# Kernel tuning notes

Hardware: AMD Instinct MI355X
Metric: run time of the kernel (lower is better)

The kernel has to match this reference:

```python
import jax, jax.numpy as jnp
import numpy as np
from functools import partial

BLUR_K = 5
SIGMA = 1.5
DOWN = 4
SCALE = 5.0
OFFSET = 0.2

_DN = ('NCHW', 'OIHW', 'NCHW')


def _gaussian_kernel(k, sigma):
    x = jnp.arange(k, dtype=jnp.float32) - (k - 1) / 2.0
    g = jnp.exp(-x ** 2 / (2.0 * sigma ** 2))
    g2 = jnp.outer(g, g)
    g2 = g2 / g2.sum()
    return g2.reshape(1, 1, k, k)


def setup_inputs() -> dict:
    key = jax.random.key(0)
    left_rgb = jax.random.uniform(key, (16, 3, 544, 960), dtype=jnp.float32)
    return {"left_rgb": left_rgb}


def reference(left_rgb):
    B, C, H, W = left_rgb.shape
    # rgb -> gray (1x1 conv with fixed weights)
    w = jnp.array([0.2989, 0.587, 0.114], dtype=left_rgb.dtype)
    gray = jnp.einsum('bchw,c->bhw', left_rgb, w)[:, None]  # [B,1,H,W]

    # gaussian blur with reflect padding (torch F.pad mode='reflect')
    pad = BLUR_K // 2
    gray_p = jnp.pad(gray, ((0, 0), (0, 0), (pad, pad), (pad, pad)), mode='reflect')
    gk = _gaussian_kernel(BLUR_K, SIGMA).astype(left_rgb.dtype)
    gray_smooth = jax.lax.conv_general_dilated(gray_p, gk, (1, 1), 'VALID',
                                               dimension_numbers=_DN)

    # sobel gradients (cross-correlation, zero padding=1, same as torch conv2d)
    sx = jnp.array([[-1., 0., 1.], [-2., 0., 2.], [-1., 0., 1.]],
                   dtype=left_rgb.dtype).reshape(1, 1, 3, 3)
    sy = jnp.array([[-1., -2., -1.], [0., 0., 0.], [1., 2., 1.]],
                   dtype=left_rgb.dtype).reshape(1, 1, 3, 3)
    gx = jax.lax.conv_general_dilated(gray_smooth, sx, (1, 1), [(1, 1), (1, 1)],
                                      dimension_numbers=_DN)
    gy = jax.lax.conv_general_dilated(gray_smooth, sy, (1, 1), [(1, 1), (1, 1)],
                                      dimension_numbers=_DN)
    mag = jnp.sqrt(gx ** 2 + gy ** 2 + 1e-6)  # [B,1,H,W]

    # avg_pool2d kernel=stride=DOWN (H, W divisible by DOWN)
    down = mag.reshape(B, 1, H // DOWN, DOWN, W // DOWN, DOWN).mean(axis=(3, 5))

    edge_mask = jax.nn.sigmoid(SCALE * (down - OFFSET)) ** 2.0
    return edge_mask
```

## Files before the change

kernel.cpp:

```cpp
#include <hip/hip_runtime.h>
#include <cmath>

constexpr int B = 16, C = 3, H = 544, W = 960;
constexpr int OH = 136, OW = 240;
constexpr size_t HW = (size_t)H * W;

constexpr int TRW = 17;
constexpr int TCW = 30;
constexpr int NTILES = B * TRW * TCW;
constexpr int WPB = 4;
constexpr int NBLK = NTILES / WPB;
constexpr int CPX = NBLK / 8;

constexpr int GRr = 38;
constexpr int GQ = 10;
constexpr int NQ = GRr * GQ;
constexpr int GS2 = 44;

__global__ __launch_bounds__(256)
void edge_wave(const float* __restrict__ in, float* __restrict__ out,
               float gn0, float gn1, float gn2)
{
    __shared__ float gray[WPB * GRr * GS2];

    const int tid  = threadIdx.x;
    const int lane = tid & 63;
    const int wv   = tid >> 6;
    const int blk  = ((int)blockIdx.x & 7) * CPX + ((int)blockIdx.x >> 3);
    const int t    = blk * WPB + wv;
    const int tc   = t % TCW;
    const int tr   = (t / TCW) % TRW;
    const int b    = t / (TCW * TRW);
    const int mh0  = tr * 32, mw0 = tc * 32;
    const float* inb = in + (size_t)b * C * HW;
    float* gw = &gray[wv * GRr * GS2];

    auto qaddr = [&](int q) -> const float* {
        const int r = q / GQ, cq = q - r * GQ;
        int g = mh0 - 3 + r;
        g = g < 0 ? -g : (g >= H ? 2 * H - 2 - g : g);
        int gcb = mw0 - 4 + 4 * cq;
        gcb = gcb < 0 ? 0 : (gcb > W - 4 ? W - 4 : gcb);
        return inb + (size_t)g * W + gcb;
    };
    auto cvt = [&](const float4& R, const float4& G, const float4& Bc) -> float4 {
        float4 g;
        g.x = fmaf(0.2989f, R.x, fmaf(0.587f, G.x, 0.114f * Bc.x));
        g.y = fmaf(0.2989f, R.y, fmaf(0.587f, G.y, 0.114f * Bc.y));
        g.z = fmaf(0.2989f, R.z, fmaf(0.587f, G.z, 0.114f * Bc.z));
        g.w = fmaf(0.2989f, R.w, fmaf(0.587f, G.w, 0.114f * Bc.w));
        return g;
    };

    {
        float4 Rv[3], Gv[3], Bv[3];
        #pragma unroll
        for (int k = 0; k < 3; ++k) {
            const float* p = qaddr(lane + 64 * k);
            Rv[k] = *reinterpret_cast<const float4*>(p);
            Gv[k] = *reinterpret_cast<const float4*>(p + HW);
            Bv[k] = *reinterpret_cast<const float4*>(p + 2 * HW);
        }
        #pragma unroll
        for (int k = 0; k < 3; ++k) {
            const int q = lane + 64 * k;
            const int r = q / GQ, cq = q - r * GQ;
            *reinterpret_cast<float4*>(&gw[r * GS2 + 4 * cq]) = cvt(Rv[k], Gv[k], Bv[k]);
        }
    }
    {
        float4 Rv[3], Gv[3], Bv[3];
        int qk[3];
        #pragma unroll
        for (int k = 0; k < 3; ++k) {
            int q = lane + 192 + 64 * k;
            qk[k] = q;
            q = q < NQ ? q : NQ - 1;
            const float* p = qaddr(q);
            Rv[k] = *reinterpret_cast<const float4*>(p);
            Gv[k] = *reinterpret_cast<const float4*>(p + HW);
            Bv[k] = *reinterpret_cast<const float4*>(p + 2 * HW);
        }
        #pragma unroll
        for (int k = 0; k < 3; ++k) {
            const int q = qk[k];
            if (q < NQ) {
                const int r = q / GQ, cq = q - r * GQ;
                *reinterpret_cast<float4*>(&gw[r * GS2 + 4 * cq]) = cvt(Rv[k], Gv[k], Bv[k]);
            }
        }
    }

    asm volatile("s_waitcnt lgkmcnt(0)" ::: "memory");
    __builtin_amdgcn_sched_barrier(0);

    if (tc == 0) {
        if (lane < GRr) {
            float* g_ = &gw[lane * GS2];
            const float4 v = make_float4(g_[8], g_[7], g_[6], g_[5]);
            *reinterpret_cast<float4*>(g_) = v;
        }
    } else if (tc == TCW - 1) {
        if (lane < GRr) {
            float* g_ = &gw[lane * GS2];
            const float4 v = make_float4(g_[34], g_[33], g_[32], g_[31]);
            *reinterpret_cast<float4*>(&g_[36]) = v;
        }
    }
    asm volatile("s_waitcnt lgkmcnt(0)" ::: "memory");
    __builtin_amdgcn_sched_barrier(0);

    __builtin_amdgcn_s_setprio(1);
    {
        const int or_ = lane >> 3;
        const int oc  = lane & 7;
        const int rb  = 4 * or_;
        const int lc0 = 4 * oc;

        float sm6[6][6];
        #pragma unroll
        for (int i = 0; i < 6; ++i)
            #pragma unroll
            for (int j = 0; j < 6; ++j) sm6[i][j] = 0.f;

        const float gk[5] = {gn0, gn1, gn2, gn1, gn0};
        #pragma unroll
        for (int t2 = 0; t2 < 10; ++t2) {
            const float* p = &gw[(rb + t2) * GS2 + lc0];
            const float4 u = *reinterpret_cast<const float4*>(p);
            const float4 v = *reinterpret_cast<const float4*>(p + 4);
            const float4 w = *reinterpret_cast<const float4*>(p + 8);
            const float t12[12] = {u.x, u.y, u.z, u.w, v.x, v.y, v.z, v.w,
                                   w.x, w.y, w.z, w.w};
            float h6[6];
            #pragma unroll
            for (int j = 0; j < 6; ++j)
                h6[j] = fmaf(gn0, t12[1 + j] + t12[5 + j],
                        fmaf(gn1, t12[2 + j] + t12[4 + j], gn2 * t12[3 + j]));
            #pragma unroll
            for (int i = 0; i < 6; ++i) {
                const int m = t2 - i;
                if (m >= 0 && m < 5) {
                    #pragma unroll
                    for (int j = 0; j < 6; ++j)
                        sm6[i][j] = fmaf(gk[m], h6[j], sm6[i][j]);
                }
            }
        }

        #pragma unroll
        for (int i = 0; i < 6; ++i) {
            const int hh = mh0 + 4 * or_ - 1 + i;
            const float rm = (hh >= 0 && hh < H) ? 1.f : 0.f;
            #pragma unroll
            for (int j = 0; j < 6; ++j) {
                const int ww = mw0 + 4 * oc - 1 + j;
                sm6[i][j] *= rm * ((ww >= 0 && ww < W) ? 1.f : 0.f);
            }
        }

        float acc[4] = {0.f, 0.f, 0.f, 0.f};
        #pragma unroll
        for (int i = 0; i < 4; ++i) {
            #pragma unroll
            for (int j = 0; j < 4; ++j) {
                const float a00 = sm6[i][j],     a01 = sm6[i][j + 1],     a02 = sm6[i][j + 2];
                const float a10 = sm6[i + 1][j],                          a12 = sm6[i + 1][j + 2];
                const float a20 = sm6[i + 2][j], a21 = sm6[i + 2][j + 1], a22 = sm6[i + 2][j + 2];
                const float gx = (a02 - a00) + 2.f * (a12 - a10) + (a22 - a20);
                const float gy = (a20 + 2.f * a21 + a22) - (a00 + 2.f * a01 + a02);
                acc[i] += sqrtf(gx * gx + gy * gy + 1e-6f);
            }
        }
        const float down = ((acc[0] + acc[1]) + (acc[2] + acc[3])) * (1.f / 16.f);
        const float x = 5.0f * (down - 0.2f);
        const float sg = 1.f / (1.f + __expf(-x));
        out[((size_t)b * OH + 8 * tr + or_) * OW + 8 * tc + oc] = sg * sg;
    }
    __builtin_amdgcn_s_setprio(0);
}

extern "C" void kernel_launch(void* const* d_in, const int* in_sizes, int n_in,
                              void* d_out, int out_size, void* d_ws, size_t ws_size,
                              hipStream_t stream) {
    const float* in = (const float*)d_in[0];
    float* out = (float*)d_out;

    const double g0 = std::exp(-4.0 / 4.5);
    const double g1 = std::exp(-1.0 / 4.5);
    const double g2 = 1.0;
    const double S = 2.0 * (g0 + g1) + g2;
    const float gn0 = (float)(g0 / S);
    const float gn1 = (float)(g1 / S);
    const float gn2 = (float)(g2 / S);

    hipLaunchKernelGGL(edge_wave, dim3(NBLK), dim3(256), 0, stream,
                       in, out, gn0, gn1, gn2);
}
```

Baseline: 31.01 us.

## Widen per-wave tile to 32x64 with two output pixels per lane

Each wave now covers a 32x64 input tile instead of 32x32, and each lane computes two horizontally adjacent pooled outputs, written as a single float2 store. The halo overhead per output shrinks, horizontal blur intermediates are shared across the two outputs, and all 11 load batches are issued before conversion, giving more memory-level parallelism. In exchange the block drops to 128 threads (2 waves), register pressure rises with the wider accumulators and 33 in-flight float4 loads, and occupancy may fall.

```diff
diff --git a/kernel.cpp b/kernel.cpp
--- a/kernel.cpp
+++ b/kernel.cpp
@@ -6,18 +6,19 @@
 constexpr size_t HW = (size_t)H * W;
 
 constexpr int TRW = 17;
-constexpr int TCW = 30;
+constexpr int TCW = 15;
 constexpr int NTILES = B * TRW * TCW;
-constexpr int WPB = 4;
+constexpr int WPB = 2;
 constexpr int NBLK = NTILES / WPB;
 constexpr int CPX = NBLK / 8;
 
 constexpr int GRr = 38;
-constexpr int GQ = 10;
+constexpr int GQ = 18;
 constexpr int NQ = GRr * GQ;
-constexpr int GS2 = 44;
+constexpr int GS2 = 76;
+constexpr int NLD = 11;
 
-__global__ __launch_bounds__(256)
+__global__ __launch_bounds__(128)
 void edge_wave(const float* __restrict__ in, float* __restrict__ out,
                float gn0, float gn1, float gn2)
 {
@@ -31,7 +32,7 @@
     const int tc   = t % TCW;
     const int tr   = (t / TCW) % TRW;
     const int b    = t / (TCW * TRW);
-    const int mh0  = tr * 32, mw0 = tc * 32;
+    const int mh0  = tr * 32, mw0 = tc * 64;
     const float* inb = in + (size_t)b * C * HW;
     float* gw = &gray[wv * GRr * GS2];
 
@@ -43,51 +44,28 @@
         gcb = gcb < 0 ? 0 : (gcb > W - 4 ? W - 4 : gcb);
         return inb + (size_t)g * W + gcb;
     };
-    auto cvt = [&](const float4& R, const float4& G, const float4& Bc) -> float4 {
-        float4 g;
-        g.x = fmaf(0.2989f, R.x, fmaf(0.587f, G.x, 0.114f * Bc.x));
-        g.y = fmaf(0.2989f, R.y, fmaf(0.587f, G.y, 0.114f * Bc.y));
-        g.z = fmaf(0.2989f, R.z, fmaf(0.587f, G.z, 0.114f * Bc.z));
-        g.w = fmaf(0.2989f, R.w, fmaf(0.587f, G.w, 0.114f * Bc.w));
-        return g;
-    };
 
-    {
-        float4 Rv[3], Gv[3], Bv[3];
-        #pragma unroll
-        for (int k = 0; k < 3; ++k) {
-            const float* p = qaddr(lane + 64 * k);
-            Rv[k] = *reinterpret_cast<const float4*>(p);
-            Gv[k] = *reinterpret_cast<const float4*>(p + HW);
-            Bv[k] = *reinterpret_cast<const float4*>(p + 2 * HW);
-        }
-        #pragma unroll
-        for (int k = 0; k < 3; ++k) {
-            const int q = lane + 64 * k;
+    float4 Rv[NLD], Gv[NLD], Bv[NLD];
+    #pragma unroll
+    for (int k = 0; k < NLD; ++k) {
+        int q = lane + 64 * k;
+        q = q < NQ ? q : NQ - 1;
+        const float* p = qaddr(q);
+        Rv[k] = *reinterpret_cast<const float4*>(p);
+        Gv[k] = *reinterpret_cast<const float4*>(p + HW);
+        Bv[k] = *reinterpret_cast<const float4*>(p + 2 * HW);
+    }
+    #pragma unroll
+    for (int k = 0; k < NLD; ++k) {
+        const int q = lane + 64 * k;
+        if (q < NQ) {
             const int r = q / GQ, cq = q - r * GQ;
-            *reinterpret_cast<float4*>(&gw[r * GS2 + 4 * cq]) = cvt(Rv[k], Gv[k], Bv[k]);
-        }
-    }
-    {
-        float4 Rv[3], Gv[3], Bv[3];
-        int qk[3];
-        #pragma unroll
-        for (int k = 0; k < 3; ++k) {
-            int q = lane + 192 + 64 * k;
-            qk[k] = q;
-            q = q < NQ ? q : NQ - 1;
-            const float* p = qaddr(q);
-            Rv[k] = *reinterpret_cast<const float4*>(p);
-            Gv[k] = *reinterpret_cast<const float4*>(p + HW);
-            Bv[k] = *reinterpret_cast<const float4*>(p + 2 * HW);
-        }
-        #pragma unroll
-        for (int k = 0; k < 3; ++k) {
-            const int q = qk[k];
-            if (q < NQ) {
-                const int r = q / GQ, cq = q - r * GQ;
-                *reinterpret_cast<float4*>(&gw[r * GS2 + 4 * cq]) = cvt(Rv[k], Gv[k], Bv[k]);
-            }
+            float4 g;
+            g.x = fmaf(0.2989f, Rv[k].x, fmaf(0.587f, Gv[k].x, 0.114f * Bv[k].x));
+            g.y = fmaf(0.2989f, Rv[k].y, fmaf(0.587f, Gv[k].y, 0.114f * Bv[k].y));
+            g.z = fmaf(0.2989f, Rv[k].z, fmaf(0.587f, Gv[k].z, 0.114f * Bv[k].z));
+            g.w = fmaf(0.2989f, Rv[k].w, fmaf(0.587f, Gv[k].w, 0.114f * Bv[k].w));
+            *reinterpret_cast<float4*>(&gw[r * GS2 + 4 * cq]) = g;
         }
     }
 
@@ -103,8 +81,8 @@
     } else if (tc == TCW - 1) {
         if (lane < GRr) {
             float* g_ = &gw[lane * GS2];
-            const float4 v = make_float4(g_[34], g_[33], g_[32], g_[31]);
-            *reinterpret_cast<float4*>(&g_[36]) = v;
+            const float4 v = make_float4(g_[66], g_[65], g_[64], g_[63]);
+            *reinterpret_cast<float4*>(&g_[68]) = v;
         }
     }
     asm volatile("s_waitcnt lgkmcnt(0)" ::: "memory");
@@ -113,15 +91,15 @@
     __builtin_amdgcn_s_setprio(1);
     {
         const int or_ = lane >> 3;
-        const int oc  = lane & 7;
+        const int ocp = lane & 7;
         const int rb  = 4 * or_;
-        const int lc0 = 4 * oc;
+        const int lc0 = 8 * ocp;
 
-        float sm6[6][6];
+        float sm6[6][10];
         #pragma unroll
         for (int i = 0; i < 6; ++i)
             #pragma unroll
-            for (int j = 0; j < 6; ++j) sm6[i][j] = 0.f;
+            for (int j = 0; j < 10; ++j) sm6[i][j] = 0.f;
 
         const float gk[5] = {gn0, gn1, gn2, gn1, gn0};
         #pragma unroll
@@ -130,20 +108,21 @@
             const float4 u = *reinterpret_cast<const float4*>(p);
             const float4 v = *reinterpret_cast<const float4*>(p + 4);
             const float4 w = *reinterpret_cast<const float4*>(p + 8);
-            const float t12[12] = {u.x, u.y, u.z, u.w, v.x, v.y, v.z, v.w,
-                                   w.x, w.y, w.z, w.w};
-            float h6[6];
+            const float4 x = *reinterpret_cast<const float4*>(p + 12);
+            const float t16[16] = {u.x, u.y, u.z, u.w, v.x, v.y, v.z, v.w,
+                                   w.x, w.y, w.z, w.w, x.x, x.y, x.z, x.w};
+            float h10[10];
             #pragma unroll
-            for (int j = 0; j < 6; ++j)
-                h6[j] = fmaf(gn0, t12[1 + j] + t12[5 + j],
-                        fmaf(gn1, t12[2 + j] + t12[4 + j], gn2 * t12[3 + j]));
+            for (int j = 0; j < 10; ++j)
+                h10[j] = fmaf(gn0, t16[1 + j] + t16[5 + j],
+                         fmaf(gn1, t16[2 + j] + t16[4 + j], gn2 * t16[3 + j]));
             #pragma unroll
             for (int i = 0; i < 6; ++i) {
                 const int m = t2 - i;
                 if (m >= 0 && m < 5) {
                     #pragma unroll
-                    for (int j = 0; j < 6; ++j)
-                        sm6[i][j] = fmaf(gk[m], h6[j], sm6[i][j]);
+                    for (int j = 0; j < 10; ++j)
+                        sm6[i][j] = fmaf(gk[m], h10[j], sm6[i][j]);
                 }
             }
         }
@@ -153,29 +132,36 @@
             const int hh = mh0 + 4 * or_ - 1 + i;
             const float rm = (hh >= 0 && hh < H) ? 1.f : 0.f;
             #pragma unroll
-            for (int j = 0; j < 6; ++j) {
-                const int ww = mw0 + 4 * oc - 1 + j;
+            for (int j = 0; j < 10; ++j) {
+                const int ww = mw0 + 8 * ocp - 1 + j;
                 sm6[i][j] *= rm * ((ww >= 0 && ww < W) ? 1.f : 0.f);
             }
         }
 
-        float acc[4] = {0.f, 0.f, 0.f, 0.f};
+        float2 o2;
         #pragma unroll
-        for (int i = 0; i < 4; ++i) {
+        for (int px = 0; px < 2; ++px) {
+            const int jb = 4 * px;
+            float acc[4] = {0.f, 0.f, 0.f, 0.f};
             #pragma unroll
-            for (int j = 0; j < 4; ++j) {
-                const float a00 = sm6[i][j],     a01 = sm6[i][j + 1],     a02 = sm6[i][j + 2];
-                const float a10 = sm6[i + 1][j],                          a12 = sm6[i + 1][j + 2];
-                const float a20 = sm6[i + 2][j], a21 = sm6[i + 2][j + 1], a22 = sm6[i + 2][j + 2];
-                const float gx = (a02 - a00) + 2.f * (a12 - a10) + (a22 - a20);
-                const float gy = (a20 + 2.f * a21 + a22) - (a00 + 2.f * a01 + a02);
-                acc[i] += sqrtf(gx * gx + gy * gy + 1e-6f);
+            for (int i = 0; i < 4; ++i) {
+                #pragma unroll
+                for (int j = 0; j < 4; ++j) {
+                    const float a00 = sm6[i][jb + j],     a01 = sm6[i][jb + j + 1],     a02 = sm6[i][jb + j + 2];
+                    const float a10 = sm6[i + 1][jb + j],                               a12 = sm6[i + 1][jb + j + 2];
+                    const float a20 = sm6[i + 2][jb + j], a21 = sm6[i + 2][jb + j + 1], a22 = sm6[i + 2][jb + j + 2];
+                    const float gx = (a02 - a00) + 2.f * (a12 - a10) + (a22 - a20);
+                    const float gy = (a20 + 2.f * a21 + a22) - (a00 + 2.f * a01 + a02);
+                    acc[i] += sqrtf(gx * gx + gy * gy + 1e-6f);
+                }
             }
+            const float down = ((acc[0] + acc[1]) + (acc[2] + acc[3])) * (1.f / 16.f);
+            const float x = 5.0f * (down - 0.2f);
+            const float sg = 1.f / (1.f + __expf(-x));
+            (px == 0 ? o2.x : o2.y) = sg * sg;
         }
-        const float down = ((acc[0] + acc[1]) + (acc[2] + acc[3])) * (1.f / 16.f);
-        const float x = 5.0f * (down - 0.2f);
-        const float sg = 1.f / (1.f + __expf(-x));
-        out[((size_t)b * OH + 8 * tr + or_) * OW + 8 * tc + oc] = sg * sg;
+        float* op = out + ((size_t)b * OH + 8 * tr + or_) * OW + 16 * tc + 2 * ocp;
+        *reinterpret_cast<float2*>(op) = o2;
     }
     __builtin_amdgcn_s_setprio(0);
 }
@@ -194,6 +180,6 @@
     const float gn1 = (float)(g1 / S);
     const float gn2 = (float)(g2 / S);
 
-    hipLaunchKernelGGL(edge_wave, dim3(NBLK), dim3(256), 0, stream,
+    hipLaunchKernelGGL(edge_wave, dim3(NBLK), dim3(128), 0, stream,
                        in, out, gn0, gn1, gn2);
 }
```

Measured after the change: 46.93 us. 1.51x slower.
